# Performance work log

Measured on AMD Instinct MI355X. Metric: run time of the kernel, lower is better.

Reference implementation:

```python
import jax, jax.numpy as jnp
from jax import lax
import numpy as np

N, D, K = 262144, 256, 32


def setup_inputs() -> dict:
    key = jax.random.key(0)
    k1, k2 = jax.random.split(key)
    inputs = jax.random.normal(k1, (N, D), dtype=jnp.float32)
    q_vectors = jax.random.normal(k2, (K, D), dtype=jnp.float32)
    return {"inputs": inputs, "q_vectors": q_vectors}


def reference(inputs, q_vectors):
    # Sequence of Householder reflections: x <- x - (x @ q) outer (2/||q||^2 q)
    squared_norms = jnp.sum(q_vectors ** 2, axis=-1)  # [K]

    def step(x, qn):
        q, sq = qn  # q: [D], sq: scalar
        coeff = x @ q  # [N]
        x = x - jnp.outer(coeff, (2.0 / sq) * q)  # rank-1 update, [N, D]
        return x, None

    outputs, _ = lax.scan(step, inputs, (q_vectors, squared_norms))
    logabsdet = jnp.zeros(inputs.shape[0], dtype=inputs.dtype)
    return outputs, logabsdet
```

## Files before the change

### kernel.cpp

```cpp
#include <hip/hip_runtime.h>

#define NROWS 262144
#define DDIM  256
#define KREF  32

template <int CTRL>
__device__ __forceinline__ float dpp_xadd(float v) {
    int r = __builtin_amdgcn_update_dpp(0, __float_as_int(v), CTRL, 0xF, 0xF, true);
    return v + __int_as_float(r);
}
__device__ __forceinline__ float reduce16(float s) {
    s = dpp_xadd<0xB1>(s);
    s = dpp_xadd<0x4E>(s);
    s = dpp_xadd<0x141>(s);
    s = dpp_xadd<0x140>(s);
    return s;
}

__global__ void beta_kernel(const float* __restrict__ q, float* __restrict__ beta) {
    int k = threadIdx.x;
    if (k < KREF) {
        const float4* row = (const float4*)(q + k * DDIM);
        float s0 = 0.f, s1 = 0.f, s2 = 0.f, s3 = 0.f;
        #pragma unroll 8
        for (int i = 0; i < DDIM / 4; ++i) {
            float4 v = row[i];
            s0 += v.x * v.x; s1 += v.y * v.y;
            s2 += v.z * v.z; s3 += v.w * v.w;
        }
        beta[k] = 2.0f / ((s0 + s1) + (s2 + s3));
    }
}

__global__ __launch_bounds__(256)
void hh_kernel(const float* __restrict__ X, const float* __restrict__ Q,
               const float* __restrict__ beta, float* __restrict__ out) {
    __shared__ float q_lds[KREF * DDIM];
    __shared__ float beta_lds[KREF];

    const int tid = threadIdx.x;

    {
        const float4* qsrc = (const float4*)Q;
        float4* qdst = (float4*)q_lds;
        #pragma unroll
        for (int i = 0; i < (KREF * DDIM / 4) / 256; ++i)
            qdst[tid + i * 256] = qsrc[tid + i * 256];
        if (tid < KREF) beta_lds[tid] = beta[tid];
    }
    __syncthreads();

    const int wave = tid >> 6;
    const int lane = tid & 63;
    const int t = lane & 15;
    const int g = lane >> 4;

    const int rbase = blockIdx.x * 64 + wave * 16;
    const int row0  = rbase + g;

    float4 x[4][4];
    #pragma unroll
    for (int j = 0; j < 4; ++j) {
        const float* rp = X + (size_t)(row0 + j * 4) * DDIM + 4 * t;
        #pragma unroll
        for (int c = 0; c < 4; ++c)
            x[j][c] = *(const float4*)(rp + c * 64);
    }

    for (int k = 0; k < KREF; ++k) {
        const float* qk = q_lds + k * DDIM + 4 * t;
        float4 qf[4];
        #pragma unroll
        for (int c = 0; c < 4; ++c)
            qf[c] = *(const float4*)(qk + c * 64);
        const float bk = beta_lds[k];

        #pragma unroll
        for (int j = 0; j < 4; ++j) {
            float s = 0.f;
            #pragma unroll
            for (int c = 0; c < 4; ++c) {
                s += x[j][c].x * qf[c].x;
                s += x[j][c].y * qf[c].y;
                s += x[j][c].z * qf[c].z;
                s += x[j][c].w * qf[c].w;
            }
            s = reduce16(s);
            const float cb = s * bk;
            #pragma unroll
            for (int c = 0; c < 4; ++c) {
                x[j][c].x -= cb * qf[c].x;
                x[j][c].y -= cb * qf[c].y;
                x[j][c].z -= cb * qf[c].z;
                x[j][c].w -= cb * qf[c].w;
            }
        }
    }

    #pragma unroll
    for (int j = 0; j < 4; ++j) {
        float* rp = out + (size_t)(row0 + j * 4) * DDIM + 4 * t;
        #pragma unroll
        for (int c = 0; c < 4; ++c)
            *(float4*)(rp + c * 64) = x[j][c];
    }

    if (tid < 64)
        out[(size_t)NROWS * DDIM + blockIdx.x * 64 + tid] = 0.0f;
}

extern "C" void kernel_launch(void* const* d_in, const int* in_sizes, int n_in,
                              void* d_out, int out_size, void* d_ws, size_t ws_size,
                              hipStream_t stream) {
    const float* X = (const float*)d_in[0];
    const float* Q = (const float*)d_in[1];
    float* out  = (float*)d_out;
    float* beta = (float*)d_ws;

    beta_kernel<<<1, 64, 0, stream>>>(Q, beta);
    hh_kernel<<<NROWS / 64, 256, 0, stream>>>(X, Q, beta, out);
}
```

Before: 473.2 us.

## Replace sequential Householder updates with compact WY form using split-bf16 MFMA

Recasts the 32 sequential rank-1 Householder reflections as the compact WY representation X - (X Q^T) T Q. A single-block setup kernel builds the Gram matrix, the triangular T factor and U = T Q. The main kernel then does two small GEMMs per 16-row tile on MFMA, splitting fp32 into bf16 hi/lo pairs (three products each) to keep roughly fp32 accuracy. This removes the 32 dependent dot-product/reduce/update passes and their DPP reductions, at the cost of a serial setup kernel, re-reading X from global in the epilogue, and reduced precision from dropping the lo*lo term.

```diff
diff --git a/kernel.cpp b/kernel.cpp
--- a/kernel.cpp
+++ b/kernel.cpp
@@ -1,112 +1,182 @@
 #include <hip/hip_runtime.h>
 
-#define NROWS 262144
-#define DDIM  256
-#define KREF  32
+#define N_ROWS 262144
+#define DDIM   256
+#define KREF   32
 
-template <int CTRL>
-__device__ __forceinline__ float dpp_xadd(float v) {
-    int r = __builtin_amdgcn_update_dpp(0, __float_as_int(v), CTRL, 0xF, 0xF, true);
-    return v + __int_as_float(r);
+typedef __attribute__((ext_vector_type(4))) float f32x4;
+typedef __attribute__((ext_vector_type(8))) short bf16x8;
+
+__device__ bf16x8 g_Vhi[2 * 8 * 64];
+__device__ bf16x8 g_Vlo[2 * 8 * 64];
+__device__ bf16x8 g_Uhi[16 * 64];
+__device__ bf16x8 g_Ulo[16 * 64];
+
+__device__ __forceinline__ unsigned short f2bf(float x) {
+    unsigned u = __float_as_uint(x);
+    u += 0x7fffu + ((u >> 16) & 1u);
+    return (unsigned short)(u >> 16);
 }
-__device__ __forceinline__ float reduce16(float s) {
-    s = dpp_xadd<0xB1>(s);
-    s = dpp_xadd<0x4E>(s);
-    s = dpp_xadd<0x141>(s);
-    s = dpp_xadd<0x140>(s);
-    return s;
+__device__ __forceinline__ float bf2f(unsigned short h) {
+    return __uint_as_float(((unsigned)h) << 16);
 }
 
-__global__ void beta_kernel(const float* __restrict__ q, float* __restrict__ beta) {
-    int k = threadIdx.x;
-    if (k < KREF) {
-        const float4* row = (const float4*)(q + k * DDIM);
-        float s0 = 0.f, s1 = 0.f, s2 = 0.f, s3 = 0.f;
-        #pragma unroll 8
-        for (int i = 0; i < DDIM / 4; ++i) {
-            float4 v = row[i];
-            s0 += v.x * v.x; s1 += v.y * v.y;
-            s2 += v.z * v.z; s3 += v.w * v.w;
+__global__ __launch_bounds__(256)
+void setup_kernel(const float* __restrict__ Q) {
+    __shared__ float G[32 * 32];
+    __shared__ float T[32 * 32];
+    __shared__ float beta[32];
+    __shared__ float U[256 * 32];
+    const int tid = threadIdx.x;
+
+    for (int p = tid; p < 1024; p += 256) {
+        const int i = p >> 5, j = p & 31;
+        const float* qi = Q + i * DDIM;
+        const float* qj = Q + j * DDIM;
+        float s = 0.f;
+        for (int d = 0; d < DDIM; ++d) s += qi[d] * qj[d];
+        G[p] = s;
+    }
+    __syncthreads();
+
+    if (tid < 32) beta[tid] = 2.0f / G[tid * 32 + tid];
+    for (int p = tid; p < 1024; p += 256) T[p] = 0.f;
+    __syncthreads();
+
+    for (int k = 0; k < 32; ++k) {
+        if (tid < k) {
+            float s = 0.f;
+            for (int j = tid; j < k; ++j) s += T[tid * 32 + j] * G[j * 32 + k];
+            T[tid * 32 + k] = -beta[k] * s;
+        } else if (tid == k) {
+            T[k * 32 + k] = beta[k];
         }
-        beta[k] = 2.0f / ((s0 + s1) + (s2 + s3));
+        __syncthreads();
+    }
+
+    for (int p = tid; p < 256 * 32; p += 256) {
+        const int d = p >> 5, k = p & 31;
+        float s = 0.f;
+        for (int j = k; j < 32; ++j) s += T[k * 32 + j] * Q[j * DDIM + d];
+        U[d * 32 + k] = s;
+    }
+    __syncthreads();
+
+    for (int e = tid; e < 2 * 8 * 64; e += 256) {
+        const int lane = e & 63, c = (e >> 6) & 7, nt = e >> 9;
+        const int q  = 16 * nt + (lane & 15);
+        const int d0 = 32 * c + 8 * (lane >> 4);
+        bf16x8 vh, vl;
+        for (int j = 0; j < 8; ++j) {
+            const float x = Q[q * DDIM + d0 + j];
+            const unsigned short h = f2bf(x);
+            vh[j] = (short)h;
+            vl[j] = (short)f2bf(x - bf2f(h));
+        }
+        g_Vhi[e] = vh; g_Vlo[e] = vl;
+    }
+    for (int e = tid; e < 16 * 64; e += 256) {
+        const int lane = e & 63, nt = e >> 6;
+        const int d  = 16 * nt + (lane & 15);
+        const int k0 = 8 * (lane >> 4);
+        bf16x8 uh, ul;
+        for (int j = 0; j < 8; ++j) {
+            const float x = U[d * 32 + k0 + j];
+            const unsigned short h = f2bf(x);
+            uh[j] = (short)h;
+            ul[j] = (short)f2bf(x - bf2f(h));
+        }
+        g_Uhi[e] = uh; g_Ulo[e] = ul;
     }
 }
 
 __global__ __launch_bounds__(256)
-void hh_kernel(const float* __restrict__ X, const float* __restrict__ Q,
-               const float* __restrict__ beta, float* __restrict__ out) {
-    __shared__ float q_lds[KREF * DDIM];
-    __shared__ float beta_lds[KREF];
+void wy_kernel(const float* __restrict__ X, float* __restrict__ out) {
+    __shared__ float tlds[4 * 16 * 36];
 
-    const int tid = threadIdx.x;
-
-    {
-        const float4* qsrc = (const float4*)Q;
-        float4* qdst = (float4*)q_lds;
-        #pragma unroll
-        for (int i = 0; i < (KREF * DDIM / 4) / 256; ++i)
-            qdst[tid + i * 256] = qsrc[tid + i * 256];
-        if (tid < KREF) beta_lds[tid] = beta[tid];
-    }
-    __syncthreads();
-
+    const int tid  = threadIdx.x;
     const int wave = tid >> 6;
     const int lane = tid & 63;
     const int t = lane & 15;
     const int g = lane >> 4;
 
-    const int rbase = blockIdx.x * 64 + wave * 16;
-    const int row0  = rbase + g;
+    const size_t row0 = (size_t)blockIdx.x * 64 + wave * 16;
 
-    float4 x[4][4];
+    const float* xp = X + (row0 + t) * DDIM + 8 * g;
+    f32x4 xa[16];
     #pragma unroll
-    for (int j = 0; j < 4; ++j) {
-        const float* rp = X + (size_t)(row0 + j * 4) * DDIM + 4 * t;
-        #pragma unroll
-        for (int c = 0; c < 4; ++c)
-            x[j][c] = *(const float4*)(rp + c * 64);
+    for (int c = 0; c < 8; ++c) {
+        xa[2 * c]     = *(const f32x4*)(xp + 32 * c);
+        xa[2 * c + 1] = *(const f32x4*)(xp + 32 * c + 4);
     }
 
-    for (int k = 0; k < KREF; ++k) {
-        const float* qk = q_lds + k * DDIM + 4 * t;
-        float4 qf[4];
+    bf16x8 ahi[8], alo[8];
+    #pragma unroll
+    for (int c = 0; c < 8; ++c) {
         #pragma unroll
-        for (int c = 0; c < 4; ++c)
-            qf[c] = *(const float4*)(qk + c * 64);
-        const float bk = beta_lds[k];
-
-        #pragma unroll
-        for (int j = 0; j < 4; ++j) {
-            float s = 0.f;
-            #pragma unroll
-            for (int c = 0; c < 4; ++c) {
-                s += x[j][c].x * qf[c].x;
-                s += x[j][c].y * qf[c].y;
-                s += x[j][c].z * qf[c].z;
-                s += x[j][c].w * qf[c].w;
-            }
-            s = reduce16(s);
-            const float cb = s * bk;
-            #pragma unroll
-            for (int c = 0; c < 4; ++c) {
-                x[j][c].x -= cb * qf[c].x;
-                x[j][c].y -= cb * qf[c].y;
-                x[j][c].z -= cb * qf[c].z;
-                x[j][c].w -= cb * qf[c].w;
-            }
+        for (int e = 0; e < 8; ++e) {
+            const float x = (e < 4) ? xa[2 * c][e] : xa[2 * c + 1][e - 4];
+            const unsigned short h = f2bf(x);
+            ahi[c][e] = (short)h;
+            alo[c][e] = (short)f2bf(x - bf2f(h));
         }
     }
 
+    f32x4 acc0 = {0.f, 0.f, 0.f, 0.f};
+    f32x4 acc1 = {0.f, 0.f, 0.f, 0.f};
     #pragma unroll
-    for (int j = 0; j < 4; ++j) {
-        float* rp = out + (size_t)(row0 + j * 4) * DDIM + 4 * t;
+    for (int c = 0; c < 8; ++c) {
+        const bf16x8 bh0 = g_Vhi[c * 64 + lane];
+        const bf16x8 bl0 = g_Vlo[c * 64 + lane];
+        const bf16x8 bh1 = g_Vhi[512 + c * 64 + lane];
+        const bf16x8 bl1 = g_Vlo[512 + c * 64 + lane];
+        acc0 = __builtin_amdgcn_mfma_f32_16x16x32_bf16(ahi[c], bh0, acc0, 0, 0, 0);
+        acc0 = __builtin_amdgcn_mfma_f32_16x16x32_bf16(alo[c], bh0, acc0, 0, 0, 0);
+        acc0 = __builtin_amdgcn_mfma_f32_16x16x32_bf16(ahi[c], bl0, acc0, 0, 0, 0);
+        acc1 = __builtin_amdgcn_mfma_f32_16x16x32_bf16(ahi[c], bh1, acc1, 0, 0, 0);
+        acc1 = __builtin_amdgcn_mfma_f32_16x16x32_bf16(alo[c], bh1, acc1, 0, 0, 0);
+        acc1 = __builtin_amdgcn_mfma_f32_16x16x32_bf16(ahi[c], bl1, acc1, 0, 0, 0);
+    }
+
+    float* tb = tlds + wave * (16 * 36);
+    #pragma unroll
+    for (int r = 0; r < 4; ++r) {
+        tb[(4 * g + r) * 36 + t]      = acc0[r];
+        tb[(4 * g + r) * 36 + 16 + t] = acc1[r];
+    }
+    asm volatile("s_waitcnt lgkmcnt(0)" ::: "memory");
+    const f32x4 c01 = *(const f32x4*)(tb + t * 36 + 8 * g);
+    const f32x4 c23 = *(const f32x4*)(tb + t * 36 + 8 * g + 4);
+
+    bf16x8 chi, clo;
+    #pragma unroll
+    for (int j = 0; j < 8; ++j) {
+        const float v = -((j < 4) ? c01[j] : c23[j - 4]);
+        const unsigned short h = f2bf(v);
+        chi[j] = (short)h;
+        clo[j] = (short)f2bf(v - bf2f(h));
+    }
+
+    const float* xr = X  + row0 * DDIM;
+    float*       op = out + row0 * DDIM;
+    #pragma unroll
+    for (int nt = 0; nt < 16; ++nt) {
+        const bf16x8 bh = g_Uhi[nt * 64 + lane];
+        const bf16x8 bl = g_Ulo[nt * 64 + lane];
+        f32x4 a = {0.f, 0.f, 0.f, 0.f};
+        a = __builtin_amdgcn_mfma_f32_16x16x32_bf16(chi, bh, a, 0, 0, 0);
+        a = __builtin_amdgcn_mfma_f32_16x16x32_bf16(clo, bh, a, 0, 0, 0);
+        a = __builtin_amdgcn_mfma_f32_16x16x32_bf16(chi, bl, a, 0, 0, 0);
+        const int col = 16 * nt + t;
         #pragma unroll
-        for (int c = 0; c < 4; ++c)
-            *(float4*)(rp + c * 64) = x[j][c];
+        for (int r = 0; r < 4; ++r) {
+            const int rr = 4 * g + r;
+            op[rr * DDIM + col] = xr[rr * DDIM + col] + a[r];
+        }
     }
 
     if (tid < 64)
-        out[(size_t)NROWS * DDIM + blockIdx.x * 64 + tid] = 0.0f;
+        out[(size_t)N_ROWS * DDIM + (size_t)blockIdx.x * 64 + tid] = 0.0f;
 }
 
 extern "C" void kernel_launch(void* const* d_in, const int* in_sizes, int n_in,
@@ -114,9 +184,8 @@
                               hipStream_t stream) {
     const float* X = (const float*)d_in[0];
     const float* Q = (const float*)d_in[1];
-    float* out  = (float*)d_out;
-    float* beta = (float*)d_ws;
+    float* out = (float*)d_out;
 
-    beta_kernel<<<1, 64, 0, stream>>>(Q, beta);
-    hh_kernel<<<NROWS / 64, 256, 0, stream>>>(X, Q, beta, out);
+    setup_kernel<<<1, 256, 0, stream>>>(Q);
+    wy_kernel<<<N_ROWS / 64, 256, 0, stream>>>(X, out);
 }
```

Measured after the change: 633.8 us. 34.0% more time.
